# Performance work log

Measured on AMD Instinct MI355X. Metric: run time of the kernel, lower is better.

Reference implementation:

```python
import jax, jax.numpy as jnp
import numpy as np

WS = 8          # window size
DISP = 4        # ws // 2 cyclic shift displacement
WS2 = WS * WS   # tokens per window
HEADS = 3
HD = 32         # head dim
SCALE = HD ** -0.5


def _mask(upper_lower, left_right):
    m = np.zeros((WS2, WS2), np.float32)
    if upper_lower:
        m[-DISP * WS:, :-DISP * WS] = -np.inf
        m[:-DISP * WS, -DISP * WS:] = -np.inf
    if left_right:
        m = m.reshape(WS, WS, WS, WS)
        m[:, -DISP:, :, :-DISP] = -np.inf
        m[:, :-DISP, :, -DISP:] = -np.inf
        m = m.reshape(WS2, WS2)
    return m

UL = _mask(True, False)
LR = _mask(False, True)
_ix = np.array([(i, j) for i in range(WS) for j in range(WS)])
REL = (_ix[None] - _ix[:, None]) + WS - 1  # [WS2, WS2, 2] relative index table


def _ln(x, g, b):
    m = x.mean(-1, keepdims=True)
    v = ((x - m) ** 2).mean(-1, keepdims=True)
    return (x - m) * jax.lax.rsqrt(v + 1e-5) * g + b


def _wattn(x, Wqkv, pos, Wo, bo, shifted):
    if shifted:
        x = jnp.roll(x, (-DISP, -DISP), axis=(1, 2))
    b, H, W, _ = x.shape
    nh, nw = H // WS, W // WS
    # qkv: last dim laid out as (3, heads, head_dim) matching torch chunk + rearrange
    qkv = (x @ Wqkv).reshape(b, nh, WS, nw, WS, 3, HEADS, HD)
    qkv = qkv.transpose(5, 0, 6, 1, 3, 2, 4, 7).reshape(3, b, HEADS, nh * nw, WS2, HD)
    q, k, v = qkv[0], qkv[1], qkv[2]
    dots = jnp.einsum('bhwid,bhwjd->bhwij', q, k) * SCALE  # [b,h,nwin,ws2,ws2]
    dots = dots + pos[REL[..., 0], REL[..., 1]]            # relative pos bias
    if shifted:
        m = np.zeros((nh * nw, WS2, WS2), np.float32)
        m[-nw:] += UL             # windows in last row
        m[nw - 1::nw] += LR       # windows in last column
        dots = dots + jnp.asarray(m)[None, None]
    a = jax.nn.softmax(dots, axis=-1)
    o = jnp.einsum('bhwij,bhwjd->bhwid', a, v)
    o = o.reshape(b, HEADS, nh, nw, WS, WS, HD).transpose(0, 2, 4, 3, 5, 1, 6).reshape(b, H, W, HEADS * HD)
    o = o @ Wo + bo
    if shifted:
        o = jnp.roll(o, (DISP, DISP), axis=(1, 2))
    return o


def _block(t, g1, b1, Wqkv, pos, Wo, bo, g2, b2, W1, bf1, W2, bf2, shifted):
    t = t + _wattn(_ln(t, g1, b1), Wqkv, pos, Wo, bo, shifted)
    h = _ln(t, g2, b2)
    return t + (jax.nn.gelu(h @ W1 + bf1, approximate=False) @ W2 + bf2)


def _stage(x, Wm, bm, pa, pb):
    b, c, H, W = x.shape
    nh, nw = H // 2, W // 2
    # PatchMerging: Unfold(k=2,s=2) layout is (c, ki, kj) with c outermost
    t = x.reshape(b, c, nh, 2, nw, 2).transpose(0, 2, 4, 1, 3, 5).reshape(b, nh, nw, c * 4)
    t = t @ Wm + bm
    t = _block(t, *pa, False)
    t = _block(t, *pb, True)
    return t.transpose(0, 3, 1, 2)


def setup_inputs() -> dict:
    key = jax.random.key(0)
    ks = jax.random.split(key, 12)
    def w(k, shp):
        return jax.random.normal(k, shp, jnp.float32) * 0.02
    def blk(kw, kp, ko, k1, k2):
        return {'g1': jnp.ones((128,), jnp.float32), 'b1': jnp.zeros((128,), jnp.float32),
                'Wqkv': w(kw, (128, 288)), 'pos': jax.random.normal(kp, (15, 15), jnp.float32),
                'Wo': w(ko, (96, 128)), 'bo': jnp.zeros((128,), jnp.float32),
                'g2': jnp.ones((128,), jnp.float32), 'b2': jnp.zeros((128,), jnp.float32),
                'W1': w(k1, (128, 512)), 'bf1': jnp.zeros((512,), jnp.float32),
                'W2': w(k2, (512, 128)), 'bf2': jnp.zeros((128,), jnp.float32)}
    A = blk(ks[2], ks[3], ks[4], ks[5], ks[6])
    B = blk(ks[7], ks[8], ks[9], ks[10], ks[11])
    inp = {'x': jax.random.normal(ks[0], (8, 64, 256, 256), jnp.float32),
           'Wm': w(ks[1], (256, 128)), 'bm': jnp.zeros((128,), jnp.float32)}
    for n, v in A.items():
        inp[n + 'a'] = v
    for n, v in B.items():
        inp[n + 'b'] = v
    return inp


def reference(x, Wm, bm, g1a, b1a, Wqkva, posa, Woa, boa, g2a, b2a, W1a, bf1a, W2a, bf2a,
              g1b, b1b, Wqkvb, posb, Wob, bob, g2b, b2b, W1b, bf1b, W2b, bf2b):
    pa = (g1a, b1a, Wqkva, posa, Woa, boa, g2a, b2a, W1a, bf1a, W2a, bf2a)
    pb = (g1b, b1b, Wqkvb, posb, Wob, bob, g2b, b2b, W1b, bf1b, W2b, bf2b)
    return _stage(x, Wm, bm, pa, pb)
```

## Files before the change

### kernel.cpp

```cpp
#include <hip/hip_runtime.h>
#include <math.h>

#define Timg 131072
#define SCALE 0.17677669529663689f

typedef __attribute__((ext_vector_type(8))) short frag8;
typedef __attribute__((ext_vector_type(8))) unsigned short us8;
typedef __attribute__((ext_vector_type(4))) float f32x4;
typedef __attribute__((ext_vector_type(4))) unsigned int u32x4;

__device__ inline float bf2f(unsigned short u) {
    union { unsigned int i; float f; } v; v.i = ((unsigned int)u) << 16; return v.f;
}
__device__ inline unsigned short f2bf(float f) {
    union { float f; unsigned int i; } v; v.f = f;
    unsigned int r = v.i + 0x7fff + ((v.i >> 16) & 1);
    return (unsigned short)(r >> 16);
}
__device__ inline unsigned int pk2(float lo, float hi) {
    return ((unsigned int)f2bf(hi) << 16) | (unsigned int)f2bf(lo);
}
__device__ inline float gelu_f(float x) {
    float u = x * x;
    float z = x * fmaf(u, 0.044715f, 1.0f);
    float e = __builtin_amdgcn_exp2f(-2.3025851f * z);
    return x * __builtin_amdgcn_rcpf(1.f + e);
}

__global__ __launch_bounds__(256) void k_wcvt(
    const float* __restrict__ src, unsigned short* __restrict__ dst, int R, int C,
    int qrows, float s)
{
    int idx = blockIdx.x * 256 + threadIdx.x;
    if (idx >= R * C) return;
    int r = idx / C, c = idx % C;
    float v = src[idx];
    if (c < qrows) v *= s;
    dst[(size_t)c * R + r] = f2bf(v);
}

#define LDA_PM 264
__global__ __launch_bounds__(256) void k_patchmerge(
    const float* __restrict__ x, const unsigned short* __restrict__ Wmt,
    const float* __restrict__ bm, float* __restrict__ t)
{
    __shared__ unsigned short A[64 * LDA_PM];
    int blk = blockIdx.x;
    int b   = blk >> 8;
    int rem = blk & 255;
    int h   = rem >> 1;
    int w0  = (rem & 1) * 64;
    int tid = threadIdx.x;
    {
        int row = tid >> 1, half = tid & 1;
        int c = row >> 1, ki = row & 1;
        const float* src = x + (((size_t)(b*64 + c))*256 + (size_t)(2*h + ki))*256 + 2*w0 + half*64;
        int base = c*4 + ki*2;
        #pragma unroll
        for (int q = 0; q < 16; ++q) {
            float4 v = *reinterpret_cast<const float4*>(src + q*4);
            int tk0 = (half*64 + q*4) >> 1;
            *reinterpret_cast<unsigned int*>(&A[ tk0     * LDA_PM + base]) = pk2(v.x, v.y);
            *reinterpret_cast<unsigned int*>(&A[(tk0 + 1)* LDA_PM + base]) = pk2(v.z, v.w);
        }
    }
    __syncthreads();
    int lane = tid & 63, w = tid >> 6;
    int lr = lane & 15, lg = lane >> 4;
    size_t tok0 = (size_t)blk * 64;
    #pragma unroll
    for (int nt = 0; nt < 2; ++nt) {
        int n0 = (w*2 + nt) * 16;
        f32x4 acc[4] = {};
        #pragma unroll
        for (int ks = 0; ks < 8; ++ks) {
            frag8 bfr = *reinterpret_cast<const frag8*>(Wmt + (size_t)(n0 + lr)*256 + ks*32 + lg*8);
            #pragma unroll
            for (int m = 0; m < 4; ++m) {
                frag8 af = *reinterpret_cast<const frag8*>(&A[(m*16 + lr)*LDA_PM + ks*32 + lg*8]);
                acc[m] = __builtin_amdgcn_mfma_f32_16x16x32_bf16(af, bfr, acc[m], 0, 0, 0);
            }
        }
        #pragma unroll
        for (int m = 0; m < 4; ++m)
            #pragma unroll
            for (int r = 0; r < 4; ++r) {
                int rowl = m*16 + lg*4 + r;
                int col  = n0 + lr;
                t[(tok0 + rowl)*128 + col] = acc[m][r] + bm[col];
            }
    }
}

#define LDQK 200
#define LDVT 72
#define LDP  72
#define LDAO 104
#define LDA  136
#define LDH  136
#define OFF_VT  25600
#define OFF_HC1 17408
#define R1SZ    39424
#define OFF_AO  48640
#define SMEMSZ  61952
__global__ __launch_bounds__(256, 2) void k_block(
    const float* __restrict__ pos, float* __restrict__ t,
    const float* __restrict__ g1, const float* __restrict__ b1,
    const unsigned short* __restrict__ Wqt,
    const unsigned short* __restrict__ Wot, const float* __restrict__ bo,
    const float* __restrict__ g2, const float* __restrict__ b2,
    const unsigned short* __restrict__ W1t, const float* __restrict__ bf1,
    const unsigned short* __restrict__ W2t, const float* __restrict__ bf2,
    int shifted)
{
    __shared__ __attribute__((aligned(16))) char smem[SMEMSZ];
    __shared__ float stats[64][4][2];
    __shared__ float ps[225];
    unsigned short* QK   = (unsigned short*)(smem);
    unsigned short* Vt   = (unsigned short*)(smem + OFF_VT);
    unsigned short* Hc0  = (unsigned short*)(smem);
    unsigned short* Hc1  = (unsigned short*)(smem + OFF_HC1);
    unsigned short* Abuf = (unsigned short*)(smem + R1SZ);
    unsigned short* P    = (unsigned short*)(smem + R1SZ);
    unsigned short* ao   = (unsigned short*)(smem + OFF_AO);

    int blk = blockIdx.x;
    int b   = blk >> 8;
    int win = blk & 255;
    int wy  = win >> 4, wx = win & 15;
    int tid = threadIdx.x, lane = tid & 63, w = tid >> 6;
    int lr  = lane & 15, lg = lane >> 4;
    int l16 = lane & 15, quad = lane >> 4;
    int sh  = shifted ? 4 : 0;

    for (int idx = tid; idx < 225; idx += 256) ps[idx] = pos[idx];

    float4 gv0 = *reinterpret_cast<const float4*>(g1 + l16*8);
    float4 gv1 = *reinterpret_cast<const float4*>(g1 + l16*8 + 4);
    float4 bv0 = *reinterpret_cast<const float4*>(b1 + l16*8);
    float4 bv1 = *reinterpret_cast<const float4*>(b1 + l16*8 + 4);
    #pragma unroll
    for (int it2 = 0; it2 < 4; ++it2) {
        int m  = w*16 + it2*4 + quad;
        int ir = m >> 3, ic = m & 7;
        int hh = (wy*8 + ir + sh) & 127, ww = (wx*8 + ic + sh) & 127;
        const float* p = t + ((size_t)((b*128 + hh)*128 + ww))*128 + l16*8;
        float4 v0 = *reinterpret_cast<const float4*>(p);
        float4 v1 = *reinterpret_cast<const float4*>(p + 4);
        float s = v0.x+v0.y+v0.z+v0.w + v1.x+v1.y+v1.z+v1.w;
        float q = v0.x*v0.x+v0.y*v0.y+v0.z*v0.z+v0.w*v0.w
                + v1.x*v1.x+v1.y*v1.y+v1.z*v1.z+v1.w*v1.w;
        #pragma unroll
        for (int o = 8; o; o >>= 1) { s += __shfl_xor(s, o); q += __shfl_xor(q, o); }
        float mean = s * 0.0078125f;
        float var  = fmaxf(q * 0.0078125f - mean*mean, 0.f);
        float rs   = rsqrtf(var + 1e-5f);
        u32x4 pk;
        pk.x = pk2((v0.x-mean)*rs*gv0.x + bv0.x, (v0.y-mean)*rs*gv0.y + bv0.y);
        pk.y = pk2((v0.z-mean)*rs*gv0.z + bv0.z, (v0.w-mean)*rs*gv0.w + bv0.w);
        pk.z = pk2((v1.x-mean)*rs*gv1.x + bv1.x, (v1.y-mean)*rs*gv1.y + bv1.y);
        pk.w = pk2((v1.z-mean)*rs*gv1.z + bv1.z, (v1.w-mean)*rs*gv1.w + bv1.w);
        *reinterpret_cast<u32x4*>(&Abuf[m*LDA + l16*8]) = pk;
    }
    __syncthreads();

    for (int nt = w; nt < 18; nt += 4) {
        f32x4 acc[4] = {};
        #pragma unroll
        for (int ks = 0; ks < 4; ++ks) {
            frag8 bfr = *reinterpret_cast<const frag8*>(Wqt + (size_t)(nt*16 + lr)*128 + ks*32 + lg*8);
            #pragma unroll
            for (int m = 0; m < 4; ++m) {
                frag8 af = *reinterpret_cast<const frag8*>(&Abuf[(m*16 + lr)*LDA + ks*32 + lg*8]);
                acc[m] = __builtin_amdgcn_mfma_f32_16x16x32_bf16(af, bfr, acc[m], 0, 0, 0);
            }
        }
        if (nt < 12) {
            #pragma unroll
            for (int m = 0; m < 4; ++m)
                #pragma unroll
                for (int r = 0; r < 4; ++r)
                    QK[(m*16 + lg*4 + r)*LDQK + nt*16 + lr] = f2bf(acc[m][r]);
        } else {
            #pragma unroll
            for (int m = 0; m < 4; ++m)
                #pragma unroll
                for (int r = 0; r < 4; ++r)
                    Vt[((nt - 12)*16 + lr)*LDVT + (m*16 + lg*4 + r)] = f2bf(acc[m][r]);
        }
    }
    __syncthreads();

    bool mUL = (shifted != 0) && (wy == 15);
    bool mLR = (shifted != 0) && (wx == 15);
    #pragma unroll 1
    for (int h = 0; h < 3; ++h) {
        frag8 qf = *reinterpret_cast<const frag8*>(&QK[(w*16 + lr)*LDQK + h*32 + lg*8]);
        f32x4 s[4];
        #pragma unroll
        for (int jt = 0; jt < 4; ++jt) {
            frag8 kf = *reinterpret_cast<const frag8*>(&QK[(jt*16 + lr)*LDQK + 96 + h*32 + lg*8]);
            f32x4 z = {0.f, 0.f, 0.f, 0.f};
            s[jt] = __builtin_amdgcn_mfma_f32_16x16x32_bf16(qf, kf, z, 0, 0, 0);
        }
        #pragma unroll
        for (int r = 0; r < 4; ++r) {
            int i  = w*16 + lg*4 + r;
            int ir = i >> 3, ic = i & 7;
            int ro = (7 - ir)*15 + (7 - ic);
            float vals[4]; float mx = -1e30f;
            #pragma unroll
            for (int jt = 0; jt < 4; ++jt) {
                int j = jt*16 + lr, jr = j >> 3, jc = j & 7;
                float val = s[jt][r] + ps[ro + jr*15 + jc];
                if ((mUL && ((jr >= 4) != (ir >= 4))) || (mLR && ((jc >= 4) != (ic >= 4)))) val = -1e30f;
                vals[jt] = val; mx = fmaxf(mx, val);
            }
            #pragma unroll
            for (int o = 8; o; o >>= 1) mx = fmaxf(mx, __shfl_xor(mx, o));
            float sum = 0.f;
            #pragma unroll
            for (int jt = 0; jt < 4; ++jt) { vals[jt] = __expf(vals[jt] - mx); sum += vals[jt]; }
            #pragma unroll
            for (int o = 8; o; o >>= 1) sum += __shfl_xor(sum, o);
            float inv = __builtin_amdgcn_rcpf(sum);
            #pragma unroll
            for (int jt = 0; jt < 4; ++jt)
                P[i*LDP + jt*16 + lr] = f2bf(vals[jt] * inv);
        }
        #pragma unroll
        for (int nd = 0; nd < 2; ++nd) {
            f32x4 o4 = {0.f, 0.f, 0.f, 0.f};
            #pragma unroll
            for (int kt = 0; kt < 2; ++kt) {
                frag8 pf = *reinterpret_cast<const frag8*>(&P[(w*16 + lr)*LDP + kt*32 + lg*8]);
                frag8 vf = *reinterpret_cast<const frag8*>(&Vt[(h*32 + nd*16 + lr)*LDVT + kt*32 + lg*8]);
                o4 = __builtin_amdgcn_mfma_f32_16x16x32_bf16(pf, vf, o4, 0, 0, 0);
            }
            #pragma unroll
            for (int r = 0; r < 4; ++r)
                ao[(w*16 + lg*4 + r)*LDAO + h*32 + nd*16 + lr] = f2bf(o4[r]);
        }
    }
    __syncthreads();

    f32x4 pacc[2][4] = {};
    #pragma unroll
    for (int ks = 0; ks < 3; ++ks) {
        frag8 bw0 = *reinterpret_cast<const frag8*>(Wot + (size_t)(w*32      + lr)*96 + ks*32 + lg*8);
        frag8 bw1 = *reinterpret_cast<const frag8*>(Wot + (size_t)(w*32 + 16 + lr)*96 + ks*32 + lg*8);
        #pragma unroll
        for (int m = 0; m < 4; ++m) {
            frag8 af = *reinterpret_cast<const frag8*>(&ao[(m*16 + lr)*LDAO + ks*32 + lg*8]);
            pacc[0][m] = __builtin_amdgcn_mfma_f32_16x16x32_bf16(af, bw0, pacc[0][m], 0, 0, 0);
            pacc[1][m] = __builtin_amdgcn_mfma_f32_16x16x32_bf16(af, bw1, pacc[1][m], 0, 0, 0);
        }
    }
    float t1[2][4][4];
    int   toks[4][4];
    #pragma unroll
    for (int m = 0; m < 4; ++m)
        #pragma unroll
        for (int r = 0; r < 4; ++r) {
            int rowl = m*16 + lg*4 + r;
            int ir = rowl >> 3, ic = rowl & 7;
            int hh = (wy*8 + ir + sh) & 127, ww = (wx*8 + ic + sh) & 127;
            toks[m][r] = (b*128 + hh)*128 + ww;
            #pragma unroll
            for (int nt = 0; nt < 2; ++nt) {
                int col = w*32 + nt*16 + lr;
                t1[nt][m][r] = t[(size_t)toks[m][r]*128 + col] + pacc[nt][m][r] + bo[col];
            }
        }
    #pragma unroll
    for (int m = 0; m < 4; ++m)
        #pragma unroll
        for (int r = 0; r < 4; ++r) {
            float v0 = t1[0][m][r], v1 = t1[1][m][r];
            float s = v0 + v1, q = v0*v0 + v1*v1;
            #pragma unroll
            for (int o = 8; o; o >>= 1) { s += __shfl_xor(s, o); q += __shfl_xor(q, o); }
            if (lr == 0) {
                int rowl = m*16 + lg*4 + r;
                stats[rowl][w][0] = s;
                stats[rowl][w][1] = q;
            }
        }
    __syncthreads();
    #pragma unroll
    for (int m = 0; m < 4; ++m)
        #pragma unroll
        for (int r = 0; r < 4; ++r) {
            int rowl = m*16 + lg*4 + r;
            float s = 0.f, q = 0.f;
            #pragma unroll
            for (int ww2 = 0; ww2 < 4; ++ww2) { s += stats[rowl][ww2][0]; q += stats[rowl][ww2][1]; }
            float mean = s * 0.0078125f;
            float var  = fmaxf(q * 0.0078125f - mean*mean, 0.f);
            float rs   = rsqrtf(var + 1e-5f);
            #pragma unroll
            for (int nt = 0; nt < 2; ++nt) {
                int col = w*32 + nt*16 + lr;
                Abuf[rowl*LDA + col] = f2bf((t1[nt][m][r] - mean)*rs*g2[col] + b2[col]);
            }
        }
    __syncthreads();

    f32x4 acc2[2][4] = {};
    #pragma unroll 1
    for (int kc = 0; kc < 4; ++kc) {
        unsigned short* Hc = (kc & 1) ? Hc1 : Hc0;
        f32x4 a1[2][4] = {};
        #pragma unroll
        for (int ks = 0; ks < 4; ++ks) {
            frag8 af[4];
            #pragma unroll
            for (int m = 0; m < 4; ++m)
                af[m] = *reinterpret_cast<const frag8*>(&Abuf[(m*16 + lr)*LDA + ks*32 + lg*8]);
            #pragma unroll
            for (int nt = 0; nt < 2; ++nt) {
                int n0 = kc*128 + w*32 + nt*16;
                frag8 bfr = *reinterpret_cast<const frag8*>(W1t + (size_t)(n0 + lr)*128 + ks*32 + lg*8);
                #pragma unroll
                for (int m = 0; m < 4; ++m)
                    a1[nt][m] = __builtin_amdgcn_mfma_f32_16x16x32_bf16(af[m], bfr, a1[nt][m], 0, 0, 0);
            }
        }
        #pragma unroll
        for (int nt = 0; nt < 2; ++nt)
            #pragma unroll
            for (int m = 0; m < 4; ++m)
                #pragma unroll
                for (int r = 0; r < 4; ++r) {
                    int rowl = m*16 + lg*4 + r;
                    int col  = w*32 + nt*16 + lr;
                    float xv = a1[nt][m][r] + bf1[kc*128 + col];
                    Hc[rowl*LDH + col] = f2bf(gelu_f(xv));
                }
        __syncthreads();
        #pragma unroll
        for (int ks = 0; ks < 4; ++ks) {
            frag8 hfk[4];
            #pragma unroll
            for (int m = 0; m < 4; ++m)
                hfk[m] = *reinterpret_cast<const frag8*>(&Hc[(m*16 + lr)*LDH + ks*32 + lg*8]);
            #pragma unroll
            for (int nt = 0; nt < 2; ++nt) {
                frag8 bfr = *reinterpret_cast<const frag8*>(W2t + (size_t)(w*32 + nt*16 + lr)*512 + kc*128 + ks*32 + lg*8);
                #pragma unroll
                for (int m = 0; m < 4; ++m)
                    acc2[nt][m] = __builtin_amdgcn_mfma_f32_16x16x32_bf16(hfk[m], bfr, acc2[nt][m], 0, 0, 0);
            }
        }
    }
    #pragma unroll
    for (int nt = 0; nt < 2; ++nt) {
        float bfv = bf2[w*32 + nt*16 + lr];
        #pragma unroll
        for (int m = 0; m < 4; ++m)
            #pragma unroll
            for (int r = 0; r < 4; ++r)
                t[(size_t)toks[m][r]*128 + w*32 + nt*16 + lr] = t1[nt][m][r] + acc2[nt][m][r] + bfv;
    }
}

__global__ __launch_bounds__(256) void k_transpose(
    const float* __restrict__ t, float* __restrict__ out)
{
    __shared__ float tile[128][33];
    int blk = blockIdx.x;
    int ct = blk & 3;
    int h  = (blk >> 2) & 127;
    int b  = blk >> 9;
    const float* src = t + ((size_t)b*16384 + (size_t)h*128)*128 + ct*32;
    #pragma unroll
    for (int q = 0; q < 16; ++q) {
        int idx = threadIdx.x + q*256;
        int w = idx >> 5, c = idx & 31;
        tile[w][c] = src[(size_t)w*128 + c];
    }
    __syncthreads();
    float* dst = out + ((size_t)(b*128 + ct*32))*16384 + (size_t)h*128;
    #pragma unroll
    for (int q = 0; q < 16; ++q) {
        int idx = threadIdx.x + q*256;
        int c = idx >> 7, w = idx & 127;
        dst[(size_t)c*16384 + w] = tile[w][c];
    }
}

extern "C" void kernel_launch(void* const* d_in, const int* in_sizes, int n_in,
                              void* d_out, int out_size, void* d_ws, size_t ws_size,
                              hipStream_t stream)
{
    const float* x  = (const float*)d_in[0];
    const float* Wm = (const float*)d_in[1];
    const float* bm = (const float*)d_in[2];

    float* t           = (float*)d_ws;
    unsigned short* wb = (unsigned short*)(t + (size_t)Timg*128);

    unsigned short* Wmt = wb;
    unsigned short* Wqt[2], *Wot[2], *W1t[2], *W2t[2];
    unsigned short* p = wb + 32768;
    for (int i = 0; i < 2; ++i) {
        Wqt[i] = p; p += 36864;
        Wot[i] = p; p += 12288;
        W1t[i] = p; p += 65536;
        W2t[i] = p; p += 65536;
    }

    k_wcvt<<<(256*128 + 255)/256, 256, 0, stream>>>(Wm, Wmt, 256, 128, 0, 1.f);
    for (int i = 0; i < 2; ++i) {
        k_wcvt<<<(128*288 + 255)/256, 256, 0, stream>>>((const float*)d_in[ 5 + i*12], Wqt[i], 128, 288, 96, SCALE);
        k_wcvt<<<( 96*128 + 255)/256, 256, 0, stream>>>((const float*)d_in[ 7 + i*12], Wot[i],  96, 128, 0, 1.f);
        k_wcvt<<<(128*512 + 255)/256, 256, 0, stream>>>((const float*)d_in[11 + i*12], W1t[i], 128, 512, 0, 1.f);
        k_wcvt<<<(512*128 + 255)/256, 256, 0, stream>>>((const float*)d_in[13 + i*12], W2t[i], 512, 128, 0, 1.f);
    }

    k_patchmerge<<<Timg/64, 256, 0, stream>>>(x, Wmt, bm, t);

    for (int blk = 0; blk < 2; ++blk) {
        const float* g1  = (const float*)d_in[ 3 + blk*12];
        const float* b1  = (const float*)d_in[ 4 + blk*12];
        const float* pos = (const float*)d_in[ 6 + blk*12];
        const float* bo  = (const float*)d_in[ 8 + blk*12];
        const float* g2  = (const float*)d_in[ 9 + blk*12];
        const float* b2  = (const float*)d_in[10 + blk*12];
        const float* bf1 = (const float*)d_in[12 + blk*12];
        const float* bf2 = (const float*)d_in[14 + blk*12];

        k_block<<<2048, 256, 0, stream>>>(pos, t, g1, b1, Wqt[blk],
                                          Wot[blk], bo, g2, b2,
                                          W1t[blk], bf1, W2t[blk], bf2, blk);
    }

    k_transpose<<<8*128*4, 256, 0, stream>>>(t, (float*)d_out);
}
```

Baseline: 388.0 us.

## Reorganize shared memory aliasing to fit three blocks per CU

Shrinks the per-block LDS footprint by overlaying buffers more aggressively: the LN output is read into registers before QK/V overwrite it, the attention outputs are held in registers until after a barrier so they can reuse the QK region, and the second LN buffer moves into the freed space. The position-bias table is also gathered straight into registers instead of being staged in shared memory. Launch bounds rise from 2 to 3 blocks per CU to raise occupancy. In exchange, register pressure grows a lot (64 A fragments plus 24 output accumulators and 16 bias values), which risks spills, and an extra barrier is added.

```diff
diff --git a/kernel.cpp b/kernel.cpp
--- a/kernel.cpp
+++ b/kernel.cpp
@@ -99,11 +99,11 @@
 #define LDA  136
 #define LDH  136
 #define OFF_VT  25600
+#define OFF_P   39424
 #define OFF_HC1 17408
-#define R1SZ    39424
-#define OFF_AO  48640
-#define SMEMSZ  61952
-__global__ __launch_bounds__(256, 2) void k_block(
+#define OFF_A2  34816
+#define SMEMSZ  52224
+__global__ __launch_bounds__(256, 3) void k_block(
     const float* __restrict__ pos, float* __restrict__ t,
     const float* __restrict__ g1, const float* __restrict__ b1,
     const unsigned short* __restrict__ Wqt,
@@ -115,14 +115,14 @@
 {
     __shared__ __attribute__((aligned(16))) char smem[SMEMSZ];
     __shared__ float stats[64][4][2];
-    __shared__ float ps[225];
-    unsigned short* QK   = (unsigned short*)(smem);
-    unsigned short* Vt   = (unsigned short*)(smem + OFF_VT);
-    unsigned short* Hc0  = (unsigned short*)(smem);
-    unsigned short* Hc1  = (unsigned short*)(smem + OFF_HC1);
-    unsigned short* Abuf = (unsigned short*)(smem + R1SZ);
-    unsigned short* P    = (unsigned short*)(smem + R1SZ);
-    unsigned short* ao   = (unsigned short*)(smem + OFF_AO);
+    unsigned short* AbufLN = (unsigned short*)(smem);
+    unsigned short* QK     = (unsigned short*)(smem);
+    unsigned short* Vt     = (unsigned short*)(smem + OFF_VT);
+    unsigned short* P      = (unsigned short*)(smem + OFF_P);
+    unsigned short* ao     = (unsigned short*)(smem);
+    unsigned short* Hc0    = (unsigned short*)(smem);
+    unsigned short* Hc1    = (unsigned short*)(smem + OFF_HC1);
+    unsigned short* A2     = (unsigned short*)(smem + OFF_A2);
 
     int blk = blockIdx.x;
     int b   = blk >> 8;
@@ -133,7 +133,17 @@
     int l16 = lane & 15, quad = lane >> 4;
     int sh  = shifted ? 4 : 0;
 
-    for (int idx = tid; idx < 225; idx += 256) ps[idx] = pos[idx];
+    float posb[4][4];
+    #pragma unroll
+    for (int r = 0; r < 4; ++r) {
+        int i  = w*16 + lg*4 + r;
+        int ir = i >> 3, ic = i & 7;
+        #pragma unroll
+        for (int jt = 0; jt < 4; ++jt) {
+            int jr = (jt*16 + lr) >> 3, jc = lr & 7;
+            posb[r][jt] = pos[(jr - ir + 7)*15 + (jc - ic + 7)];
+        }
+    }
 
     float4 gv0 = *reinterpret_cast<const float4*>(g1 + l16*8);
     float4 gv1 = *reinterpret_cast<const float4*>(g1 + l16*8 + 4);
@@ -160,8 +170,16 @@
         pk.y = pk2((v0.z-mean)*rs*gv0.z + bv0.z, (v0.w-mean)*rs*gv0.w + bv0.w);
         pk.z = pk2((v1.x-mean)*rs*gv1.x + bv1.x, (v1.y-mean)*rs*gv1.y + bv1.y);
         pk.w = pk2((v1.z-mean)*rs*gv1.z + bv1.z, (v1.w-mean)*rs*gv1.w + bv1.w);
-        *reinterpret_cast<u32x4*>(&Abuf[m*LDA + l16*8]) = pk;
-    }
+        *reinterpret_cast<u32x4*>(&AbufLN[m*LDA + l16*8]) = pk;
+    }
+    __syncthreads();
+
+    frag8 afq[4][4];
+    #pragma unroll
+    for (int ks = 0; ks < 4; ++ks)
+        #pragma unroll
+        for (int m = 0; m < 4; ++m)
+            afq[ks][m] = *reinterpret_cast<const frag8*>(&AbufLN[(m*16 + lr)*LDA + ks*32 + lg*8]);
     __syncthreads();
 
     for (int nt = w; nt < 18; nt += 4) {
@@ -170,10 +188,8 @@
         for (int ks = 0; ks < 4; ++ks) {
             frag8 bfr = *reinterpret_cast<const frag8*>(Wqt + (size_t)(nt*16 + lr)*128 + ks*32 + lg*8);
             #pragma unroll
-            for (int m = 0; m < 4; ++m) {
-                frag8 af = *reinterpret_cast<const frag8*>(&Abuf[(m*16 + lr)*LDA + ks*32 + lg*8]);
-                acc[m] = __builtin_amdgcn_mfma_f32_16x16x32_bf16(af, bfr, acc[m], 0, 0, 0);
-            }
+            for (int m = 0; m < 4; ++m)
+                acc[m] = __builtin_amdgcn_mfma_f32_16x16x32_bf16(afq[ks][m], bfr, acc[m], 0, 0, 0);
         }
         if (nt < 12) {
             #pragma unroll
@@ -193,7 +209,8 @@
 
     bool mUL = (shifted != 0) && (wy == 15);
     bool mLR = (shifted != 0) && (wx == 15);
-    #pragma unroll 1
+    f32x4 oreg[3][2];
+    #pragma unroll
     for (int h = 0; h < 3; ++h) {
         frag8 qf = *reinterpret_cast<const frag8*>(&QK[(w*16 + lr)*LDQK + h*32 + lg*8]);
         f32x4 s[4];
@@ -207,12 +224,11 @@
         for (int r = 0; r < 4; ++r) {
             int i  = w*16 + lg*4 + r;
             int ir = i >> 3, ic = i & 7;
-            int ro = (7 - ir)*15 + (7 - ic);
             float vals[4]; float mx = -1e30f;
             #pragma unroll
             for (int jt = 0; jt < 4; ++jt) {
                 int j = jt*16 + lr, jr = j >> 3, jc = j & 7;
-                float val = s[jt][r] + ps[ro + jr*15 + jc];
+                float val = s[jt][r] + posb[r][jt];
                 if ((mUL && ((jr >= 4) != (ir >= 4))) || (mLR && ((jc >= 4) != (ic >= 4)))) val = -1e30f;
                 vals[jt] = val; mx = fmaxf(mx, val);
             }
@@ -237,11 +253,18 @@
                 frag8 vf = *reinterpret_cast<const frag8*>(&Vt[(h*32 + nd*16 + lr)*LDVT + kt*32 + lg*8]);
                 o4 = __builtin_amdgcn_mfma_f32_16x16x32_bf16(pf, vf, o4, 0, 0, 0);
             }
+            oreg[h][nd] = o4;
+        }
+    }
+    __syncthreads();
+
+    #pragma unroll
+    for (int h = 0; h < 3; ++h)
+        #pragma unroll
+        for (int nd = 0; nd < 2; ++nd)
             #pragma unroll
             for (int r = 0; r < 4; ++r)
-                ao[(w*16 + lg*4 + r)*LDAO + h*32 + nd*16 + lr] = f2bf(o4[r]);
-        }
-    }
+                ao[(w*16 + lg*4 + r)*LDAO + h*32 + nd*16 + lr] = f2bf(oreg[h][nd][r]);
     __syncthreads();
 
     f32x4 pacc[2][4] = {};
@@ -301,7 +324,7 @@
             #pragma unroll
             for (int nt = 0; nt < 2; ++nt) {
                 int col = w*32 + nt*16 + lr;
-                Abuf[rowl*LDA + col] = f2bf((t1[nt][m][r] - mean)*rs*g2[col] + b2[col]);
+                A2[rowl*LDA + col] = f2bf((t1[nt][m][r] - mean)*rs*g2[col] + b2[col]);
             }
         }
     __syncthreads();
@@ -316,7 +339,7 @@
             frag8 af[4];
             #pragma unroll
             for (int m = 0; m < 4; ++m)
-                af[m] = *reinterpret_cast<const frag8*>(&Abuf[(m*16 + lr)*LDA + ks*32 + lg*8]);
+                af[m] = *reinterpret_cast<const frag8*>(&A2[(m*16 + lr)*LDA + ks*32 + lg*8]);
             #pragma unroll
             for (int nt = 0; nt < 2; ++nt) {
                 int n0 = kc*128 + w*32 + nt*16;
```

Result: slower. 438.6 us (+13.0%).
